# Kernel tuning notes

Measured on AMD Instinct MI355X. Metric: run time of the kernel, lower is better.

Reference implementation:

```python
import jax, jax.numpy as jnp
import numpy as np

B, T, D = 2, 2048, 512
H = 8
DH = D // H
DECAY = 0.99
SCALE = DH ** -0.5
NEG = -1e30

_J6 = jnp.array([[0, 0, 0, 0, 0, 1], [0, 0, 0, 0, -1, 0], [0, 0, 0, 1, 0, 0],
                 [0, 0, 1, 0, 0, 0], [0, -1, 0, 0, 0, 0], [1, 0, 0, 0, 0, 0]],
                dtype=jnp.float32)
_PAIRS4 = [(0, 1), (0, 2), (0, 3), (1, 2), (1, 3), (2, 3)]


def exterior(p1, p2):
    # p1, p2: [..., 4] -> normalized Plucker line coords [..., 6]
    parts = [p1[..., i] * p2[..., j] - p1[..., j] * p2[..., i] for i, j in _PAIRS4]
    L = jnp.stack(parts, axis=-1)
    n = jnp.sqrt(jnp.sum(L * L, axis=-1, keepdims=True))
    return L / jnp.maximum(n, 1e-12)


def setup_inputs() -> dict:
    key = jax.random.key(0)
    ks = jax.random.split(key, 16)
    s = 0.02
    return {
        "x": jax.random.normal(ks[0], (B, T, D), jnp.float32),
        "qkv_w": jax.random.normal(ks[1], (3 * D, D), jnp.float32) * s,
        "qkv_b": jnp.zeros((3 * D,), jnp.float32),
        "w1_write": jax.random.normal(ks[2], (4 * H, D), jnp.float32) * s,
        "w2_write": jax.random.normal(ks[3], (4 * H, D), jnp.float32) * s,
        "w1_read": jax.random.normal(ks[4], (4 * H, D), jnp.float32) * s,
        "w2_read": jax.random.normal(ks[5], (4 * H, D), jnp.float32) * s,
        "mem_value_w": jax.random.normal(ks[6], (D, D), jnp.float32) * s,
        "mem_value_b": jnp.zeros((D,), jnp.float32),
        "mem_gate_w": jax.random.normal(ks[7], (H, D), jnp.float32) * s,
        "mem_gate_b": jnp.zeros((H,), jnp.float32),
        "mem_scale": jnp.full((H,), 0.1, jnp.float32),
        "out_w": jax.random.normal(ks[8], (D, D), jnp.float32) * s,
        "out_b": jnp.zeros((D,), jnp.float32),
    }


def reference(x, qkv_w, qkv_b, w1_write, w2_write, w1_read, w2_read,
              mem_value_w, mem_value_b, mem_gate_w, mem_gate_b, mem_scale,
              out_w, out_b):
    b, t, d = x.shape
    # --- standard causal attention (dropout in eval mode = identity) ---
    qkv = (x @ qkv_w.T + qkv_b).reshape(b, t, 3, H, DH)
    qkv = jnp.transpose(qkv, (2, 0, 3, 1, 4))  # [3,B,H,T,dh]
    q, k, v = qkv[0], qkv[1], qkv[2]
    scores = jnp.einsum('bhtd,bhsd->bhts', q, k) * SCALE
    i = jnp.arange(t)
    upper = i[:, None] < i[None, :]  # strictly upper -> masked
    scores = jnp.where(upper, NEG, scores)
    attn = jax.nn.softmax(scores, axis=-1)
    seq_out = jnp.einsum('bhts,bhsd->bhtd', attn, v)
    seq_out = jnp.transpose(seq_out, (0, 2, 1, 3)).reshape(b, t, d)
    # --- exterior-algebra Gram memory ---
    x_prev = jnp.concatenate([jnp.zeros((b, 1, d), x.dtype), x[:, :-1]], axis=1)
    w1 = (x_prev @ w1_write.T).reshape(b, t, H, 4)
    w2 = (x @ w2_write.T).reshape(b, t, H, 4)
    write_lines = exterior(w1, w2)  # [B,T,H,6]
    r1 = (x @ w1_read.T).reshape(b, t, H, 4)
    r2 = (x @ w2_read.T).reshape(b, t, H, 4)
    read_lines = exterior(r1, r2)  # [B,T,H,6]
    J_write = jnp.einsum('bthi,ij->bthj', write_lines, _J6)
    # incidence[b,h,i,j] = <read_i, J write_j>
    incidence = jnp.einsum('bihk,bjhk->bhij', read_lines, J_write)  # [B,H,T,T]
    # decay weights, strictly lower triangular (j < i); also acts as causal mask
    pos = jnp.arange(t, dtype=x.dtype)
    delta = pos[:, None] - pos[None, :]
    weights = jnp.where(delta > 0, jnp.power(jnp.asarray(DECAY, x.dtype), delta), 0.0)
    mem_score = jnp.sum((incidence * incidence) * weights[None, None], axis=-1)  # [B,H,T]
    # --- gating ---
    mem_val = x @ mem_value_w.T + mem_value_b  # [B,T,D]
    gate = jax.nn.sigmoid(x @ mem_gate_w.T + mem_gate_b)  # [B,T,H]
    mem_score_t = jnp.transpose(mem_score, (0, 2, 1))  # [B,T,H]
    gated = jax.nn.sigmoid(mem_score_t * mem_scale[None, None, :]) * gate
    gated = jnp.mean(gated, axis=-1, keepdims=True)  # [B,T,1]
    return (seq_out + gated * mem_val) @ out_w.T + out_b
```

## Files before the change

### kernel.cpp

```cpp
#include <hip/hip_runtime.h>
#include <math.h>

#define B_ 2
#define T_ 2048
#define D_ 512
#define H_ 8
#define DH_ 64
#define SCALE_ 0.125f
#define DECAY_ 0.99f

static constexpr size_t QSZ = (size_t)B_ * H_ * T_ * DH_;

typedef __bf16 bf16x8 __attribute__((ext_vector_type(8)));
typedef float f32x4 __attribute__((ext_vector_type(4)));

__device__ inline ushort f2bf(float f) {
  uint u = __float_as_uint(f);
  u += 0x7FFF + ((u >> 16) & 1);
  return (ushort)(u >> 16);
}

__device__ inline float bf2f(ushort v) {
  return __uint_as_float(((uint)v) << 16);
}

__device__ __forceinline__ void gload16(const ushort* g, ushort* l) {
  __builtin_amdgcn_global_load_lds(
      (const __attribute__((address_space(1))) void*)g,
      (__attribute__((address_space(3))) void*)l, 16, 0, 0);
}

__global__ __launch_bounds__(256) void cast_bf16_kernel(
    const float* __restrict__ x, const float* __restrict__ qkvw,
    const float* __restrict__ mvw, const float* __restrict__ ow,
    const float* __restrict__ w1w, const float* __restrict__ w2w,
    const float* __restrict__ w1r, const float* __restrict__ w2r,
    const float* __restrict__ mgw, ushort* __restrict__ dst)
{
  size_t e0 = ((size_t)blockIdx.x * 256 + threadIdx.x) * 8;
  const float* src = nullptr;
  if (e0 < 2097152)      src = x + e0;
  else if (e0 < 2883584) src = qkvw + (e0 - 2097152);
  else if (e0 < 3145728) src = mvw + (e0 - 2883584);
  else if (e0 < 3276800) {
    size_t off = e0 - 3145728;
    int row = (int)(off >> 9), col = (int)(off & 511);
    if (row < 32)       src = w1w + (size_t)row * 512 + col;
    else if (row < 64)  src = w2w + (size_t)(row - 32) * 512 + col;
    else if (row < 96)  src = w1r + (size_t)(row - 64) * 512 + col;
    else if (row < 128) src = w2r + (size_t)(row - 96) * 512 + col;
    else if (row < 136) src = mgw + (size_t)(row - 128) * 512 + col;
    else src = nullptr;
  } else if (e0 < 3538944) src = ow + (e0 - 3276800);
  ushort tmp[8];
  if (src) {
    float4 a = *(const float4*)(src);
    float4 b = *(const float4*)(src + 4);
    tmp[0] = f2bf(a.x); tmp[1] = f2bf(a.y); tmp[2] = f2bf(a.z); tmp[3] = f2bf(a.w);
    tmp[4] = f2bf(b.x); tmp[5] = f2bf(b.y); tmp[6] = f2bf(b.z); tmp[7] = f2bf(b.w);
  } else {
#pragma unroll
    for (int i = 0; i < 8; i++) tmp[i] = 0;
  }
  *(uint4*)(dst + e0) = *(uint4*)tmp;
}

template<int EPI>
__global__ __launch_bounds__(256) void mfma_gemm(const ushort* __restrict__ A,
    const ushort* __restrict__ W, const float* __restrict__ bias,
    const float* __restrict__ bias2, void* __restrict__ Cout,
    ushort* __restrict__ memval16, float* __restrict__ proj, int M, int N, int K)
{
  __shared__ __align__(16) ushort As[128 * 64];
  __shared__ __align__(16) ushort Ws[64 * 64];
  const int tid = threadIdx.x;
  const int wave = tid >> 6, lane = tid & 63;
  const int col16 = lane & 15, grp = lane >> 4;
  const int wr = wave >> 1, wc = wave & 1;
  const int gx = gridDim.x;
  const int nwg = gx * gridDim.y;
  const int p = blockIdx.y * gx + blockIdx.x;
  const int wg = (p & 7) * (nwg >> 3) + (p >> 3);
  const int bm = (wg / gx) * 128, bn = (wg % gx) * 64;

  f32x4 acc[4][2] = {};
  const int lrow = lane >> 3, lcol = (lane & 7) * 8;

  for (int k0 = 0; k0 < K; k0 += 64) {
    __syncthreads();
#pragma unroll
    for (int i = 0; i < 4; i++) {
      int q = i * 4 + wave;
      gload16(A + (size_t)(bm + q * 8 + lrow) * K + k0 + lcol, &As[q * 512]);
    }
#pragma unroll
    for (int i = 0; i < 2; i++) {
      int q = i * 4 + wave;
      gload16(W + (size_t)(bn + q * 8 + lrow) * K + k0 + lcol, &Ws[q * 512]);
    }
    __syncthreads();
#pragma unroll
    for (int kk = 0; kk < 2; kk++) {
      bf16x8 a[4], b[2];
#pragma unroll
      for (int m = 0; m < 4; m++)
        a[m] = *(const bf16x8*)&As[(wr * 64 + m * 16 + col16) * 64 + kk * 32 + grp * 8];
#pragma unroll
      for (int n = 0; n < 2; n++)
        b[n] = *(const bf16x8*)&Ws[(wc * 32 + n * 16 + col16) * 64 + kk * 32 + grp * 8];
#pragma unroll
      for (int m = 0; m < 4; m++)
#pragma unroll
        for (int n = 0; n < 2; n++)
          acc[m][n] = __builtin_amdgcn_mfma_f32_16x16x32_bf16(a[m], b[n], acc[m][n], 0, 0, 0);
    }
  }

  if (EPI == 1) {
    ushort* q16 = (ushort*)Cout;
    ushort* k16 = q16 + QSZ;
    ushort* vt  = q16 + 2 * QSZ;
    const int sec = bn >> 9;
    if (sec == 2) {
#pragma unroll
      for (int n = 0; n < 2; n++) {
        int col = bn + wc * 32 + n * 16 + col16;
        float bv = bias[col];
        int h = (col >> 6) & 7, dh = col & 63;
#pragma unroll
        for (int m = 0; m < 4; m++) {
          int row0 = bm + wr * 64 + m * 16 + grp * 4;
          int b = row0 >> 11, t0 = row0 & 2047;
          ushort tmp4[4];
#pragma unroll
          for (int r = 0; r < 4; r++) tmp4[r] = f2bf(acc[m][n][r] + bv);
          *(uint2*)(vt + ((size_t)(b * H_ + h) * 64 + dh) * T_ + t0) = *(uint2*)tmp4;
        }
      }
    } else {
#pragma unroll
      for (int n = 0; n < 2; n++) {
        int col = bn + wc * 32 + n * 16 + col16;
        float bv;
        if (sec < 2)       bv = bias[col];
        else if (sec == 3) bv = bias2[col - 1536];
        else               bv = 0.f;
        int h = (col >> 6) & 7, dh = col & 63;
#pragma unroll
        for (int m = 0; m < 4; m++) {
#pragma unroll
          for (int r = 0; r < 4; r++) {
            int row = bm + wr * 64 + m * 16 + grp * 4 + r;
            int b = row >> 11, t = row & 2047;
            float val = acc[m][n][r] + bv;
            size_t bh = (size_t)(b * H_ + h);
            if (sec == 0)      q16[(bh * T_ + t) * 64 + dh] = f2bf(val * (SCALE_ * 1.44269504f));
            else if (sec == 1) k16[(bh * T_ + t) * 64 + dh] = f2bf(val);
            else if (sec == 3) memval16[(size_t)row * 512 + (col - 1536)] = f2bf(val);
            else               proj[(size_t)row * 256 + (col - 2048)] = val;
          }
        }
      }
    }
  } else {
    float* C = (float*)Cout;
#pragma unroll
    for (int n = 0; n < 2; n++) {
      int col = bn + wc * 32 + n * 16 + col16;
      float bv = bias[col];
#pragma unroll
      for (int m = 0; m < 4; m++) {
#pragma unroll
        for (int r = 0; r < 4; r++) {
          int row = bm + wr * 64 + m * 16 + grp * 4 + r;
          C[(size_t)row * N + col] = acc[m][n][r] + bv;
        }
      }
    }
  }
}

__global__ __launch_bounds__(256) void lines_kernel(
    const float* __restrict__ proj, const float* __restrict__ gb,
    float* __restrict__ u_out, float* __restrict__ r_out, float* __restrict__ gate_out)
{
  int gid = blockIdx.x * 256 + threadIdx.x;
  int bt = gid >> 3, h = gid & 7;
  int b = bt >> 11, t = bt & 2047;
  const float* pr = proj + (size_t)bt * 256;
  const int pi[6] = {0, 0, 0, 1, 1, 2};
  const int pj[6] = {1, 2, 3, 2, 3, 3};
  float p1[4], p2[4];
#pragma unroll
  for (int e = 0; e < 4; e++) {
    p1[e] = (t == 0) ? 0.f : proj[(size_t)(bt - 1) * 256 + h * 4 + e];
    p2[e] = pr[32 + h * 4 + e];
  }
  float L[6], n2 = 0.f;
#pragma unroll
  for (int e = 0; e < 6; e++) {
    L[e] = p1[pi[e]] * p2[pj[e]] - p1[pj[e]] * p2[pi[e]];
    n2 = fmaf(L[e], L[e], n2);
  }
  float inv = 1.f / fmaxf(sqrtf(n2), 1e-12f);
  size_t base = (((size_t)(b * H_ + h)) * T_ + t) * 6;
  u_out[base + 0] =  L[5] * inv;
  u_out[base + 1] = -L[4] * inv;
  u_out[base + 2] =  L[3] * inv;
  u_out[base + 3] =  L[2] * inv;
  u_out[base + 4] = -L[1] * inv;
  u_out[base + 5] =  L[0] * inv;
#pragma unroll
  for (int e = 0; e < 4; e++) {
    p1[e] = pr[64 + h * 4 + e];
    p2[e] = pr[96 + h * 4 + e];
  }
  n2 = 0.f;
#pragma unroll
  for (int e = 0; e < 6; e++) {
    L[e] = p1[pi[e]] * p2[pj[e]] - p1[pj[e]] * p2[pi[e]];
    n2 = fmaf(L[e], L[e], n2);
  }
  inv = 1.f / fmaxf(sqrtf(n2), 1e-12f);
#pragma unroll
  for (int e = 0; e < 6; e++) r_out[base + e] = L[e] * inv;
  gate_out[(size_t)bt * H_ + h] = 1.f / (1.f + __expf(-(pr[128 + h] + gb[h])));
}

__global__ __launch_bounds__(128) void memscore3_kernel(
    const float* __restrict__ u, const float* __restrict__ r, float* __restrict__ score)
{
  const int bh = blockIdx.x;
  const int c = blockIdx.y;
  const int tid = threadIdx.x;
  const int base = c << 7;
  const int jmax = base + 128;
  __shared__ float us_t[6][2048];
  __shared__ float red[128][25];

  const float* ug = u + (size_t)bh * T_ * 6;
  for (int idx = tid; idx < jmax * 6; idx += 128) {
    int j = idx / 6;
    int cmp = idx - j * 6;
    us_t[cmp][j] = ug[idx];
  }
  __syncthreads();

  float g[21];
#pragma unroll
  for (int q2 = 0; q2 < 21; q2++) g[q2] = 0.f;
  if (c > 0) {
    float w = __powf(DECAY_, (float)(128 - tid));
    const float d128 = 0.27624712f;
    for (int j = base - 128 + tid; j >= 0; j -= 128) {
      float u0 = us_t[0][j], u1 = us_t[1][j], u2 = us_t[2][j];
      float u3 = us_t[3][j], u4 = us_t[4][j], u5 = us_t[5][j];
      float w0 = w * u0, w1 = w * u1, w2 = w * u2, w3 = w * u3, w4 = w * u4;
      g[0] = fmaf(w0, u0, g[0]);  g[1] = fmaf(w0, u1, g[1]);
      g[2] = fmaf(w0, u2, g[2]);  g[3] = fmaf(w0, u3, g[3]);
      g[4] = fmaf(w0, u4, g[4]);  g[5] = fmaf(w0, u5, g[5]);
      g[6] = fmaf(w1, u1, g[6]);  g[7] = fmaf(w1, u2, g[7]);
      g[8] = fmaf(w1, u3, g[8]);  g[9] = fmaf(w1, u4, g[9]);
      g[10] = fmaf(w1, u5, g[10]); g[11] = fmaf(w2, u2, g[11]);
      g[12] = fmaf(w2, u3, g[12]); g[13] = fmaf(w2, u4, g[13]);
      g[14] = fmaf(w2, u5, g[14]); g[15] = fmaf(w3, u3, g[15]);
      g[16] = fmaf(w3, u4, g[16]); g[17] = fmaf(w3, u5, g[17]);
      g[18] = fmaf(w4, u4, g[18]); g[19] = fmaf(w4, u5, g[19]);
      g[20] = fmaf(w * u5, u5, g[20]);
      w *= d128;
    }
  }
#pragma unroll
  for (int q2 = 0; q2 < 21; q2++) red[tid][q2] = g[q2];
  __syncthreads();
  for (int off = 64; off > 0; off >>= 1) {
    if (tid < off) {
#pragma unroll
      for (int q2 = 0; q2 < 21; q2++) red[tid][q2] += red[tid + off][q2];
    }
    __syncthreads();
  }
  float M21[21];
#pragma unroll
  for (int q2 = 0; q2 < 21; q2++) M21[q2] = red[0][q2];

  const int i = base + tid;
  const float* ri = r + ((size_t)bh * T_ + i) * 6;
  float r0 = ri[0], r1 = ri[1], r2 = ri[2], r3 = ri[3], r4 = ri[4], r5 = ri[5];
  float q = M21[0] * r0 * r0 + M21[6] * r1 * r1 + M21[11] * r2 * r2
          + M21[15] * r3 * r3 + M21[18] * r4 * r4 + M21[20] * r5 * r5
          + 2.f * (M21[1] * r0 * r1 + M21[2] * r0 * r2 + M21[3] * r0 * r3
                 + M21[4] * r0 * r4 + M21[5] * r0 * r5 + M21[7] * r1 * r2
                 + M21[8] * r1 * r3 + M21[9] * r1 * r4 + M21[10] * r1 * r5
                 + M21[12] * r2 * r3 + M21[13] * r2 * r4 + M21[14] * r2 * r5
                 + M21[16] * r3 * r4 + M21[17] * r3 * r5 + M21[19] * r4 * r5);
  float wl = __powf(DECAY_, (float)tid);
  float sum = q * wl;
  float w = wl;
  const float invd = 1.0f / DECAY_;
  const int sbound = tid | 63;
  for (int s = 0; s < sbound; ++s) {
    float d = r0 * us_t[0][base + s] + r1 * us_t[1][base + s]
            + r2 * us_t[2][base + s] + r3 * us_t[3][base + s]
            + r4 * us_t[4][base + s] + r5 * us_t[5][base + s];
    if (s < tid) sum = fmaf(w, d * d, sum);
    w *= invd;
  }
  score[(size_t)bh * T_ + i] = sum;
}

__global__ __launch_bounds__(256) void gfac_kernel(
    const float* __restrict__ score, const float* __restrict__ gate,
    const float* __restrict__ mem_scale, float* __restrict__ gfac)
{
  int bt = blockIdx.x * 256 + threadIdx.x;
  int b = bt >> 11, t = bt & 2047;
  float acc = 0.f;
#pragma unroll
  for (int h = 0; h < H_; h++) {
    float ms = score[((size_t)(b * H_ + h)) * T_ + t];
    float sg = 1.f / (1.f + __expf(-ms * mem_scale[h]));
    acc += sg * gate[(size_t)bt * H_ + h];
  }
  gfac[bt] = acc * (1.0f / H_);
}

__global__ __launch_bounds__(256) void attn_v3_kernel(
    const ushort* __restrict__ q16, const ushort* __restrict__ k16,
    const ushort* __restrict__ vt16, const ushort* __restrict__ memval16,
    const float* __restrict__ gfac, ushort* __restrict__ seqo16)
{
  const int blk = blockIdx.x;
  const int bh = blk & 15;
  const int rg = 63 - (blk >> 4);
  const int tid = threadIdx.x;
  const int w = tid >> 6, lane = tid & 63;
  const int col16 = lane & 15, grp = lane >> 4;

  __shared__ __align__(16) ushort smemU[25600];
  ushort* vt_lds = &smemU[w * 4096];
  ushort* ps_w   = &smemU[16384 + w * 32 * 72];
  float*  combf  = (float*)smemU;

  const int i0 = rg * 32;
  const ushort* qp0 = q16 + ((size_t)bh * T_ + i0 + col16) * 64 + grp * 8;
  bf16x8 aq[2][2];
  aq[0][0] = *(const bf16x8*)(qp0);
  aq[0][1] = *(const bf16x8*)(qp0 + 32);
  aq[1][0] = *(const bf16x8*)(qp0 + 16 * 64);
  aq[1][1] = *(const bf16x8*)(qp0 + 16 * 64 + 32);

  f32x4 o[2][4] = {};
  float lsum[2][4] = {};

  const ushort* kb = k16 + (size_t)bh * T_ * 64;
  const ushort* vb = vt16 + (size_t)bh * 64 * T_;
  const int vrow = lane >> 3;
  const int vchk = ((lane & 7) ^ vrow) << 3;

  const int ntiles = (rg >> 1) + 1;
  if (w < ntiles) {
    const int j0 = w * 64;
#pragma unroll
    for (int g = 0; g < 8; g++)
      gload16(vb + (size_t)(g * 8 + vrow) * T_ + j0 + vchk, vt_lds + g * 512);
  }

  for (int kt = w; kt < ntiles; kt += 4) {
    const int j0 = kt * 64;
    f32x4 facc[2][4] = {};
#pragma unroll
    for (int jt = 0; jt < 4; jt++) {
      const ushort* kp = kb + (size_t)(j0 + jt * 16 + col16) * 64 + grp * 8;
      bf16x8 b0 = *(const bf16x8*)kp;
      bf16x8 b1 = *(const bf16x8*)(kp + 32);
#pragma unroll
      for (int rr = 0; rr < 2; rr++) {
        facc[rr][jt] = __builtin_amdgcn_mfma_f32_16x16x32_bf16(aq[rr][0], b0, facc[rr][jt], 0, 0, 0);
        facc[rr][jt] = __builtin_amdgcn_mfma_f32_16x16x32_bf16(aq[rr][1], b1, facc[rr][jt], 0, 0, 0);
      }
    }
    const bool lastt = (kt == ntiles - 1);
#pragma unroll
    for (int rr = 0; rr < 2; rr++)
#pragma unroll
      for (int jt = 0; jt < 4; jt++) {
        int j = j0 + jt * 16 + col16;
#pragma unroll
        for (int r = 0; r < 4; r++) {
          int i = i0 + rr * 16 + grp * 4 + r;
          float pv = (lastt && j > i) ? 0.f : exp2f(facc[rr][jt][r]);
          lsum[rr][r] += pv;
          ps_w[(rr * 16 + grp * 4 + r) * 72 + jt * 16 + col16] = f2bf(pv);
        }
      }
    asm volatile("s_waitcnt vmcnt(0)" ::: "memory");
#pragma unroll
    for (int ks2 = 0; ks2 < 2; ks2++)
#pragma unroll
      for (int rr = 0; rr < 2; rr++) {
        bf16x8 a = *(const bf16x8*)&ps_w[(rr * 16 + col16) * 72 + ks2 * 32 + grp * 8];
#pragma unroll
        for (int n = 0; n < 4; n++) {
          int d = n * 16 + col16;
          int cs = (ks2 * 4 + grp) ^ (col16 & 7);
          bf16x8 bv = *(const bf16x8*)&vt_lds[d * 64 + cs * 8];
          o[rr][n] = __builtin_amdgcn_mfma_f32_16x16x32_bf16(a, bv, o[rr][n], 0, 0, 0);
        }
      }
    __builtin_amdgcn_sched_barrier(0);
    if (kt + 4 < ntiles) {
      const int jn = (kt + 4) * 64;
#pragma unroll
      for (int g = 0; g < 8; g++)
        gload16(vb + (size_t)(g * 8 + vrow) * T_ + jn + vchk, vt_lds + g * 512);
    }
  }

  __syncthreads();
  if (w > 0) {
    float* dst = &combf[((w - 1) * 64 + lane) * 40];
#pragma unroll
    for (int rr = 0; rr < 2; rr++)
#pragma unroll
      for (int n = 0; n < 4; n++)
        *(float4*)&dst[(rr * 4 + n) * 4] = *(float4*)&o[rr][n];
    *(float4*)&dst[32] = make_float4(lsum[0][0], lsum[0][1], lsum[0][2], lsum[0][3]);
    *(float4*)&dst[36] = make_float4(lsum[1][0], lsum[1][1], lsum[1][2], lsum[1][3]);
  }
  __syncthreads();
  if (w == 0) {
#pragma unroll
    for (int ww = 0; ww < 3; ww++) {
      const float* src = &combf[(ww * 64 + lane) * 40];
#pragma unroll
      for (int rr = 0; rr < 2; rr++)
#pragma unroll
        for (int n = 0; n < 4; n++) {
          float4 v = *(const float4*)&src[(rr * 4 + n) * 4];
          o[rr][n][0] += v.x; o[rr][n][1] += v.y; o[rr][n][2] += v.z; o[rr][n][3] += v.w;
        }
      float4 l0 = *(const float4*)&src[32];
      float4 l1 = *(const float4*)&src[36];
      lsum[0][0] += l0.x; lsum[0][1] += l0.y; lsum[0][2] += l0.z; lsum[0][3] += l0.w;
      lsum[1][0] += l1.x; lsum[1][1] += l1.y; lsum[1][2] += l1.z; lsum[1][3] += l1.w;
    }
#pragma unroll
    for (int rr = 0; rr < 2; rr++)
#pragma unroll
      for (int r = 0; r < 4; r++) {
        float s = lsum[rr][r];
#pragma unroll
        for (int s2 = 1; s2 < 16; s2 <<= 1) s += __shfl_xor(s, s2);
        lsum[rr][r] = s;
      }
    const int b = bh >> 3, h = bh & 7;
#pragma unroll
    for (int rr = 0; rr < 2; rr++)
#pragma unroll
      for (int r = 0; r < 4; r++) {
        float inv = 1.f / lsum[rr][r];
        int i = i0 + rr * 16 + grp * 4 + r;
        float gf = gfac[b * T_ + i];
        size_t rowbase = ((size_t)(b * T_) + i) * D_ + h * 64;
#pragma unroll
        for (int n = 0; n < 4; n++) {
          int d = n * 16 + col16;
          float mv = bf2f(memval16[rowbase + d]);
          seqo16[rowbase + d] = f2bf(fmaf(gf, mv, o[rr][n][r] * inv));
        }
      }
  }
}

extern "C" void kernel_launch(void* const* d_in, const int* in_sizes, int n_in,
                              void* d_out, int out_size, void* d_ws, size_t ws_size,
                              hipStream_t stream) {
  const float* x     = (const float*)d_in[0];
  const float* qkvw  = (const float*)d_in[1];
  const float* qkvb  = (const float*)d_in[2];
  const float* w1w   = (const float*)d_in[3];
  const float* w2w   = (const float*)d_in[4];
  const float* w1r   = (const float*)d_in[5];
  const float* w2r   = (const float*)d_in[6];
  const float* mvw   = (const float*)d_in[7];
  const float* mvb   = (const float*)d_in[8];
  const float* mgw   = (const float*)d_in[9];
  const float* mgb   = (const float*)d_in[10];
  const float* mscl  = (const float*)d_in[11];
  const float* ow    = (const float*)d_in[12];
  const float* ob    = (const float*)d_in[13];
  (void)in_sizes; (void)n_in; (void)out_size; (void)ws_size;

  float* f = (float*)d_ws;
  float* proj   = f;
  float* ul     = proj + 1048576;
  float* rl     = ul + 196608;
  float* gatep  = rl + 196608;
  float* msc    = gatep + 32768;
  float* gfac   = msc + 32768;
  ushort* x16    = (ushort*)(gfac + 4096);
  ushort* wbig16 = x16 + 2097152;
  ushort* ow16   = wbig16 + 1179648;
  ushort* q16    = ow16 + 262144;
  ushort* k16    = q16 + QSZ;
  ushort* vt16   = k16 + QSZ;
  ushort* memval16 = vt16 + QSZ;
  ushort* seqo16 = x16;

  const int M = B_ * T_;

  cast_bf16_kernel<<<dim3(1728), 256, 0, stream>>>(x, qkvw, mvw, ow,
                                                   w1w, w2w, w1r, w2r, mgw, x16);
  mfma_gemm<1><<<dim3(36, 32), 256, 0, stream>>>(x16, wbig16, qkvb, mvb, q16,
                                                 memval16, proj, M, 2304, D_);
  lines_kernel<<<dim3(128), 256, 0, stream>>>(proj, mgb, ul, rl, gatep);
  memscore3_kernel<<<dim3(16, 16), 128, 0, stream>>>(ul, rl, msc);
  gfac_kernel<<<dim3(16), 256, 0, stream>>>(msc, gatep, mscl, gfac);
  attn_v3_kernel<<<dim3(16 * 64), 256, 0, stream>>>(q16, k16, vt16, memval16,
                                                    gfac, seqo16);
  mfma_gemm<0><<<dim3(8, 32), 256, 0, stream>>>(seqo16, ow16, ob, nullptr, d_out,
                                                nullptr, nullptr, M, D_, D_);
}
```

Measured before the change: 111.8 us.

## Keep attention probabilities in registers via transposed MFMA and permuted V layout

The attention kernel now computes S^T by swapping the MFMA operands, so each lane's score outputs line up with the B-operand layout of the PV MFMA. The probabilities are packed to bf16 with v_cvt_pk_bf16_f32 and fed straight into the PV product, removing the per-wave LDS staging of P and the LDS staging of V. To make this work, the QKV GEMM epilogue writes V^T with a permuted token order so direct global bf16x8 loads match the packed P fragment. The output is accumulated transposed, row sums reduce with two shuffles, and the epilogue stores four contiguous values. The cost is more global V loads per wave, with no async prefetch overlapping them.

```diff
diff --git a/kernel.cpp b/kernel.cpp
--- a/kernel.cpp
+++ b/kernel.cpp
@@ -28,6 +28,12 @@
   __builtin_amdgcn_global_load_lds(
       (const __attribute__((address_space(1))) void*)g,
       (__attribute__((address_space(3))) void*)l, 16, 0, 0);
+}
+
+__device__ __forceinline__ uint cvtpk(float lo, float hi) {
+  uint r;
+  asm("v_cvt_pk_bf16_f32 %0, %1, %2" : "=v"(r) : "v"(lo), "v"(hi));
+  return r;
 }
 
 __global__ __launch_bounds__(256) void cast_bf16_kernel(
@@ -131,10 +137,12 @@
         for (int m = 0; m < 4; m++) {
           int row0 = bm + wr * 64 + m * 16 + grp * 4;
           int b = row0 >> 11, t0 = row0 & 2047;
+          int tq = (t0 & ~63) + ((t0 >> 5) & 1) * 32 + ((t0 >> 2) & 3) * 8
+                 + ((t0 >> 4) & 1) * 4;
           ushort tmp4[4];
 #pragma unroll
           for (int r = 0; r < 4; r++) tmp4[r] = f2bf(acc[m][n][r] + bv);
-          *(uint2*)(vt + ((size_t)(b * H_ + h) * 64 + dh) * T_ + t0) = *(uint2*)tmp4;
+          *(uint2*)(vt + ((size_t)(b * H_ + h) * 64 + dh) * T_ + tq) = *(uint2*)tmp4;
         }
       }
     } else {
@@ -325,9 +333,9 @@
   gfac[bt] = acc * (1.0f / H_);
 }
 
-__global__ __launch_bounds__(256) void attn_v3_kernel(
+__global__ __launch_bounds__(256) void attn_v4_kernel(
     const ushort* __restrict__ q16, const ushort* __restrict__ k16,
-    const ushort* __restrict__ vt16, const ushort* __restrict__ memval16,
+    const ushort* __restrict__ vtp16, const ushort* __restrict__ memval16,
     const float* __restrict__ gfac, ushort* __restrict__ seqo16)
 {
   const int blk = blockIdx.x;
@@ -337,10 +345,7 @@
   const int w = tid >> 6, lane = tid & 63;
   const int col16 = lane & 15, grp = lane >> 4;
 
-  __shared__ __align__(16) ushort smemU[25600];
-  ushort* vt_lds = &smemU[w * 4096];
-  ushort* ps_w   = &smemU[16384 + w * 32 * 72];
-  float*  combf  = (float*)smemU;
+  __shared__ __align__(16) float comb[3][64][40];
 
   const int i0 = rg * 32;
   const ushort* qp0 = q16 + ((size_t)bh * T_ + i0 + col16) * 64 + grp * 8;
@@ -350,25 +355,24 @@
   aq[1][0] = *(const bf16x8*)(qp0 + 16 * 64);
   aq[1][1] = *(const bf16x8*)(qp0 + 16 * 64 + 32);
 
-  f32x4 o[2][4] = {};
-  float lsum[2][4] = {};
+  f32x4 ot[2][4] = {};
+  float lsum[2] = {0.f, 0.f};
 
   const ushort* kb = k16 + (size_t)bh * T_ * 64;
-  const ushort* vb = vt16 + (size_t)bh * 64 * T_;
-  const int vrow = lane >> 3;
-  const int vchk = ((lane & 7) ^ vrow) << 3;
+  const ushort* vb = vtp16 + (size_t)bh * 64 * T_;
 
   const int ntiles = (rg >> 1) + 1;
-  if (w < ntiles) {
-    const int j0 = w * 64;
-#pragma unroll
-    for (int g = 0; g < 8; g++)
-      gload16(vb + (size_t)(g * 8 + vrow) * T_ + j0 + vchk, vt_lds + g * 512);
-  }
-
   for (int kt = w; kt < ntiles; kt += 4) {
     const int j0 = kt * 64;
-    f32x4 facc[2][4] = {};
+    bf16x8 vf[2][4];
+#pragma unroll
+    for (int ks = 0; ks < 2; ks++)
+#pragma unroll
+      for (int n4 = 0; n4 < 4; n4++)
+        vf[ks][n4] = *(const bf16x8*)(vb + (size_t)(n4 * 16 + col16) * T_ +
+                                      j0 + ks * 32 + grp * 8);
+    const bool lastt = (kt == ntiles - 1);
+    uint pk[2][4][2];
 #pragma unroll
     for (int jt = 0; jt < 4; jt++) {
       const ushort* kp = kb + (size_t)(j0 + jt * 16 + col16) * 64 + grp * 8;
@@ -376,100 +380,84 @@
       bf16x8 b1 = *(const bf16x8*)(kp + 32);
 #pragma unroll
       for (int rr = 0; rr < 2; rr++) {
-        facc[rr][jt] = __builtin_amdgcn_mfma_f32_16x16x32_bf16(aq[rr][0], b0, facc[rr][jt], 0, 0, 0);
-        facc[rr][jt] = __builtin_amdgcn_mfma_f32_16x16x32_bf16(aq[rr][1], b1, facc[rr][jt], 0, 0, 0);
+        f32x4 facc = {};
+        facc = __builtin_amdgcn_mfma_f32_16x16x32_bf16(b0, aq[rr][0], facc, 0, 0, 0);
+        facc = __builtin_amdgcn_mfma_f32_16x16x32_bf16(b1, aq[rr][1], facc, 0, 0, 0);
+        const int i = i0 + rr * 16 + col16;
+        float p[4];
+#pragma unroll
+        for (int r = 0; r < 4; r++) {
+          int j = j0 + jt * 16 + grp * 4 + r;
+          p[r] = (lastt && j > i) ? 0.f : exp2f(facc[r]);
+          lsum[rr] += p[r];
+        }
+        pk[rr][jt][0] = cvtpk(p[0], p[1]);
+        pk[rr][jt][1] = cvtpk(p[2], p[3]);
       }
     }
-    const bool lastt = (kt == ntiles - 1);
+#pragma unroll
+    for (int ks = 0; ks < 2; ks++)
+#pragma unroll
+      for (int rr = 0; rr < 2; rr++) {
+        uint pf_u[4] = {pk[rr][2 * ks][0], pk[rr][2 * ks][1],
+                        pk[rr][2 * ks + 1][0], pk[rr][2 * ks + 1][1]};
+        bf16x8 pf = *(bf16x8*)pf_u;
+#pragma unroll
+        for (int n4 = 0; n4 < 4; n4++)
+          ot[rr][n4] = __builtin_amdgcn_mfma_f32_16x16x32_bf16(vf[ks][n4], pf, ot[rr][n4], 0, 0, 0);
+      }
+  }
+
+#pragma unroll
+  for (int rr = 0; rr < 2; rr++) {
+    lsum[rr] += __shfl_xor(lsum[rr], 16);
+    lsum[rr] += __shfl_xor(lsum[rr], 32);
+  }
+
+  if (w > 0) {
+    float* dst = &comb[w - 1][lane][0];
 #pragma unroll
     for (int rr = 0; rr < 2; rr++)
 #pragma unroll
-      for (int jt = 0; jt < 4; jt++) {
-        int j = j0 + jt * 16 + col16;
-#pragma unroll
-        for (int r = 0; r < 4; r++) {
-          int i = i0 + rr * 16 + grp * 4 + r;
-          float pv = (lastt && j > i) ? 0.f : exp2f(facc[rr][jt][r]);
-          lsum[rr][r] += pv;
-          ps_w[(rr * 16 + grp * 4 + r) * 72 + jt * 16 + col16] = f2bf(pv);
-        }
-      }
-    asm volatile("s_waitcnt vmcnt(0)" ::: "memory");
-#pragma unroll
-    for (int ks2 = 0; ks2 < 2; ks2++)
-#pragma unroll
-      for (int rr = 0; rr < 2; rr++) {
-        bf16x8 a = *(const bf16x8*)&ps_w[(rr * 16 + col16) * 72 + ks2 * 32 + grp * 8];
-#pragma unroll
-        for (int n = 0; n < 4; n++) {
-          int d = n * 16 + col16;
-          int cs = (ks2 * 4 + grp) ^ (col16 & 7);
-          bf16x8 bv = *(const bf16x8*)&vt_lds[d * 64 + cs * 8];
-          o[rr][n] = __builtin_amdgcn_mfma_f32_16x16x32_bf16(a, bv, o[rr][n], 0, 0, 0);
-        }
-      }
-    __builtin_amdgcn_sched_barrier(0);
-    if (kt + 4 < ntiles) {
-      const int jn = (kt + 4) * 64;
-#pragma unroll
-      for (int g = 0; g < 8; g++)
-        gload16(vb + (size_t)(g * 8 + vrow) * T_ + jn + vchk, vt_lds + g * 512);
-    }
-  }
-
-  __syncthreads();
-  if (w > 0) {
-    float* dst = &combf[((w - 1) * 64 + lane) * 40];
-#pragma unroll
-    for (int rr = 0; rr < 2; rr++)
-#pragma unroll
-      for (int n = 0; n < 4; n++)
-        *(float4*)&dst[(rr * 4 + n) * 4] = *(float4*)&o[rr][n];
-    *(float4*)&dst[32] = make_float4(lsum[0][0], lsum[0][1], lsum[0][2], lsum[0][3]);
-    *(float4*)&dst[36] = make_float4(lsum[1][0], lsum[1][1], lsum[1][2], lsum[1][3]);
+      for (int n4 = 0; n4 < 4; n4++)
+        *(float4*)&dst[(rr * 4 + n4) * 4] = *(float4*)&ot[rr][n4];
+    dst[32] = lsum[0];
+    dst[33] = lsum[1];
   }
   __syncthreads();
   if (w == 0) {
 #pragma unroll
     for (int ww = 0; ww < 3; ww++) {
-      const float* src = &combf[(ww * 64 + lane) * 40];
+      const float* src = &comb[ww][lane][0];
 #pragma unroll
       for (int rr = 0; rr < 2; rr++)
 #pragma unroll
-        for (int n = 0; n < 4; n++) {
-          float4 v = *(const float4*)&src[(rr * 4 + n) * 4];
-          o[rr][n][0] += v.x; o[rr][n][1] += v.y; o[rr][n][2] += v.z; o[rr][n][3] += v.w;
+        for (int n4 = 0; n4 < 4; n4++) {
+          float4 v = *(const float4*)&src[(rr * 4 + n4) * 4];
+          ot[rr][n4][0] += v.x; ot[rr][n4][1] += v.y;
+          ot[rr][n4][2] += v.z; ot[rr][n4][3] += v.w;
         }
-      float4 l0 = *(const float4*)&src[32];
-      float4 l1 = *(const float4*)&src[36];
-      lsum[0][0] += l0.x; lsum[0][1] += l0.y; lsum[0][2] += l0.z; lsum[0][3] += l0.w;
-      lsum[1][0] += l1.x; lsum[1][1] += l1.y; lsum[1][2] += l1.z; lsum[1][3] += l1.w;
-    }
-#pragma unroll
-    for (int rr = 0; rr < 2; rr++)
-#pragma unroll
-      for (int r = 0; r < 4; r++) {
-        float s = lsum[rr][r];
-#pragma unroll
-        for (int s2 = 1; s2 < 16; s2 <<= 1) s += __shfl_xor(s, s2);
-        lsum[rr][r] = s;
+      lsum[0] += src[32];
+      lsum[1] += src[33];
+    }
+    const int b = bh >> 3, h = bh & 7;
+#pragma unroll
+    for (int rr = 0; rr < 2; rr++) {
+      const int i = i0 + rr * 16 + col16;
+      const float inv = 1.f / lsum[rr];
+      const float gf = gfac[b * T_ + i];
+      const size_t rowbase = ((size_t)(b * T_) + i) * D_ + h * 64 + grp * 4;
+#pragma unroll
+      for (int n4 = 0; n4 < 4; n4++) {
+        ushort tmp4[4];
+#pragma unroll
+        for (int r = 0; r < 4; r++) {
+          float mv = bf2f(memval16[rowbase + n4 * 16 + r]);
+          tmp4[r] = f2bf(fmaf(gf, mv, ot[rr][n4][r] * inv));
+        }
+        *(uint2*)(seqo16 + rowbase + n4 * 16) = *(uint2*)tmp4;
       }
-    const int b = bh >> 3, h = bh & 7;
-#pragma unroll
-    for (int rr = 0; rr < 2; rr++)
-#pragma unroll
-      for (int r = 0; r < 4; r++) {
-        float inv = 1.f / lsum[rr][r];
-        int i = i0 + rr * 16 + grp * 4 + r;
-        float gf = gfac[b * T_ + i];
-        size_t rowbase = ((size_t)(b * T_) + i) * D_ + h * 64;
-#pragma unroll
-        for (int n = 0; n < 4; n++) {
-          int d = n * 16 + col16;
-          float mv = bf2f(memval16[rowbase + d]);
-          seqo16[rowbase + d] = f2bf(fmaf(gf, mv, o[rr][n][r] * inv));
-        }
-      }
+    }
   }
 }
 
@@ -517,7 +505,7 @@
   lines_kernel<<<dim3(128), 256, 0, stream>>>(proj, mgb, ul, rl, gatep);
   memscore3_kernel<<<dim3(16, 16), 128, 0, stream>>>(ul, rl, msc);
   gfac_kernel<<<dim3(16), 256, 0, stream>>>(msc, gatep, mscl, gfac);
-  attn_v3_kernel<<<dim3(16 * 64), 256, 0, stream>>>(q16, k16, vt16, memval16,
+  attn_v4_kernel<<<dim3(16 * 64), 256, 0, stream>>>(q16, k16, vt16, memval16,
                                                     gfac, seqo16);
   mfma_gemm<0><<<dim3(8, 32), 256, 0, stream>>>(seqo16, ow16, ob, nullptr, d_out,
                                                 nullptr, nullptr, M, D_, D_);
```

After: 111.3 us. About the same (-0.5%).
